# Kernel optimization log

Measured on AMD Instinct MI355X. Metric: run time of the kernel, lower is better.

The kernel has to match this reference:

```python
import jax, jax.numpy as jnp
import numpy as np

DIM = 64
SHAPE = (1, DIM, 12, 12, 12)  # B, C, D, H, W


def setup_inputs() -> dict:
    key = jax.random.key(0)
    k1, k2, k3, k4 = jax.random.split(key, 4)
    x = jax.random.normal(k1, SHAPE, dtype=jnp.float32)
    # torch nn.Linear weights: [out, in]; scale like default init
    w_qkv = jax.random.normal(k2, (3 * DIM, DIM), dtype=jnp.float32) * (1.0 / np.sqrt(DIM))
    w_proj = jax.random.normal(k3, (DIM, DIM), dtype=jnp.float32) * (1.0 / np.sqrt(DIM))
    b_proj = jax.random.normal(k4, (DIM,), dtype=jnp.float32) * 0.01
    return {"x": x, "w_qkv": w_qkv, "w_proj": w_proj, "b_proj": b_proj}


def reference(x, w_qkv, w_proj, b_proj):
    B, C, D, H, W = x.shape
    num_heads = C // 2  # head_dim = 2, per module definition
    head_dim = C // num_heads
    scale = head_dim ** (-0.5)
    N = D * H * W

    # [B, N, C] token layout (permute channels last, flatten spatial)
    xt = jnp.transpose(x, (0, 2, 3, 4, 1)).reshape(B, N, C)
    qkv = xt @ w_qkv.T  # [B, N, 3C]
    qkv = qkv.reshape(B, N, 3, num_heads, head_dim).transpose(2, 0, 3, 1, 4)
    q, k, v = qkv[0], qkv[1], qkv[2]  # each [B, h, N, d]

    attn = jnp.einsum('bhqd,bhkd->bhqk', q, k) * scale  # materialized scores
    attn = jax.nn.softmax(attn, axis=-1)
    out = jnp.einsum('bhqk,bhkd->bhqd', attn, v)  # [B, h, N, d]
    out = out.transpose(0, 2, 1, 3).reshape(B, D, H, W, C)
    out = out @ w_proj.T + b_proj  # [B, D, H, W, C]
    return out
```

## Files before the change

### kernel.cpp

```cpp
#include <hip/hip_runtime.h>
#include <hip/hip_bf16.h>

#define N_TOK  1728
#define CDIM   64
#define NHEADS 32
#define QTILES 27
#define NPAIR  (N_TOK / 2)
#define SCALE  0.70710678118654752f
#define LOG2E  1.44269504088896340736f
#define JW     8
#define PCH    (NPAIR / JW)

typedef _Float16 h2 __attribute__((ext_vector_type(2)));
union H2U { h2 h; unsigned int u; };

__device__ __forceinline__ unsigned int pack2(float a, float b) {
    H2U c; c.h.x = (_Float16)a; c.h.y = (_Float16)b; return c.u;
}
__device__ __forceinline__ float hdot2(unsigned int q, unsigned int k) {
    H2U a, b; a.u = q; b.u = k;
#if __has_builtin(__builtin_amdgcn_fdot2)
    return __builtin_amdgcn_fdot2(a.h, b.h, 0.0f, false);
#else
    return fmaf((float)a.h.x, (float)b.h.x, (float)a.h.y * (float)b.h.y);
#endif
}

__device__ __forceinline__ float ldin(const void* p, int i, int f32) {
    if (f32) return ((const float*)p)[i];
    union { unsigned int b; float f; } c;
    c.b = ((unsigned int)((const unsigned short*)p)[i]) << 16;
    return c.f;
}
__device__ __forceinline__ int sniff_f32(const void* x) {
    union { unsigned int b; float f; } c;
    c.b = ((unsigned int)((const unsigned short*)x)[threadIdx.x & 63]) << 16;
    int bad = (((c.b >> 23) & 0xFF) == 0xFF) || (fabsf(c.f) > 1e10f);
    return (__ballot(bad) != 0ULL) ? 1 : 0;
}

__global__ void __launch_bounds__(64)
qkv_pack(const void* __restrict__ xv, const void* __restrict__ wv,
         unsigned int* __restrict__ Qp, unsigned int* __restrict__ KVg) {
    const int f     = sniff_f32(xv);
    const int lane  = threadIdx.x;
    const int h     = blockIdx.y & 31;
    const int which = blockIdx.y >> 5;
    const int r0    = (which << 6) + 2 * h;
    const int n     = blockIdx.x * 64 + lane;
    float a0 = 0.f, a1 = 0.f;
    if (f) {
        const float* x  = (const float*)xv;
        const float* w0 = (const float*)wv + r0 * CDIM;
        const float* w1 = w0 + CDIM;
#pragma unroll 8
        for (int c = 0; c < CDIM; ++c) {
            float xc = x[c * N_TOK + n];
            a0 = fmaf(xc, w0[c], a0);
            a1 = fmaf(xc, w1[c], a1);
        }
    } else {
#pragma unroll 8
        for (int c = 0; c < CDIM; ++c) {
            float xc = ldin(xv, c * N_TOK + n, 0);
            a0 = fmaf(xc, ldin(wv, r0 * CDIM + c, 0), a0);
            a1 = fmaf(xc, ldin(wv, (r0 + 1) * CDIM + c, 0), a1);
        }
    }
    if (which == 0)
        Qp[h * N_TOK + n] = pack2(a0 * (SCALE * LOG2E), a1 * (SCALE * LOG2E));
    else
        KVg[(h * NPAIR + (n >> 1)) * 4 + ((which == 1) ? 0 : 2) + (n & 1)] =
            pack2(a0, a1);
}

__global__ void __launch_bounds__(512, 4)
attn_kernel(const unsigned int* __restrict__ Qp, const uint4* __restrict__ KVg,
            float* __restrict__ O) {
    __shared__ uint4 KVs[NPAIR];
    __shared__ float redbuf[JW * 64 * 3];
    const int tid  = threadIdx.x;
    const int lane = tid & 63;
    const int wav  = tid >> 6;
    const int h    = blockIdx.y;
    const int t0   = blockIdx.x * 64;

    const uint4* src = KVg + h * NPAIR;
    KVs[tid] = src[tid];
    if (tid < NPAIR - 512) KVs[512 + tid] = src[512 + tid];
    const unsigned int qh = Qp[h * N_TOK + t0 + lane];
    __syncthreads();

    const uint4* KVp = &KVs[wav * PCH];
    float l0 = 0.f, l1 = 0.f, l2 = 0.f, l3 = 0.f;
    float p0 = 0.f, p1 = 0.f, p2 = 0.f, p3 = 0.f;
    float s0 = 0.f, s1 = 0.f, s2 = 0.f, s3 = 0.f;
    for (int g = 0; g < PCH; g += 4) {
        uint4 d0 = KVp[g], d1 = KVp[g + 1], d2 = KVp[g + 2], d3 = KVp[g + 3];
        H2U v;
        float ea, eb;
        ea = __builtin_amdgcn_exp2f(hdot2(qh, d0.x));
        eb = __builtin_amdgcn_exp2f(hdot2(qh, d0.y));
        v.u = d0.z; l0 += ea; p0 = fmaf(ea, (float)v.h.x, p0); s0 = fmaf(ea, (float)v.h.y, s0);
        v.u = d0.w; l0 += eb; p0 = fmaf(eb, (float)v.h.x, p0); s0 = fmaf(eb, (float)v.h.y, s0);
        ea = __builtin_amdgcn_exp2f(hdot2(qh, d1.x));
        eb = __builtin_amdgcn_exp2f(hdot2(qh, d1.y));
        v.u = d1.z; l1 += ea; p1 = fmaf(ea, (float)v.h.x, p1); s1 = fmaf(ea, (float)v.h.y, s1);
        v.u = d1.w; l1 += eb; p1 = fmaf(eb, (float)v.h.x, p1); s1 = fmaf(eb, (float)v.h.y, s1);
        ea = __builtin_amdgcn_exp2f(hdot2(qh, d2.x));
        eb = __builtin_amdgcn_exp2f(hdot2(qh, d2.y));
        v.u = d2.z; l2 += ea; p2 = fmaf(ea, (float)v.h.x, p2); s2 = fmaf(ea, (float)v.h.y, s2);
        v.u = d2.w; l2 += eb; p2 = fmaf(eb, (float)v.h.x, p2); s2 = fmaf(eb, (float)v.h.y, s2);
        ea = __builtin_amdgcn_exp2f(hdot2(qh, d3.x));
        eb = __builtin_amdgcn_exp2f(hdot2(qh, d3.y));
        v.u = d3.z; l3 += ea; p3 = fmaf(ea, (float)v.h.x, p3); s3 = fmaf(ea, (float)v.h.y, s3);
        v.u = d3.w; l3 += eb; p3 = fmaf(eb, (float)v.h.x, p3); s3 = fmaf(eb, (float)v.h.y, s3);
    }
    float* red = redbuf + wav * 192 + lane * 3;
    red[0] = (l0 + l1) + (l2 + l3);
    red[1] = (p0 + p1) + (p2 + p3);
    red[2] = (s0 + s1) + (s2 + s3);
    __syncthreads();
    if (wav == 0) {
        float L = 0.f, A = 0.f, B = 0.f;
#pragma unroll
        for (int w = 0; w < JW; ++w) {
            const float* r = redbuf + w * 192 + lane * 3;
            L += r[0]; A += r[1]; B += r[2];
        }
        float inv = 1.0f / L;
        int n = t0 + lane;
        *((float2*)(O + n * CDIM + 2 * h)) = make_float2(A * inv, B * inv);
    }
}

__global__ void __launch_bounds__(256)
proj_kernel(const void* __restrict__ xv,
            const float* __restrict__ O,
            const void* __restrict__ w_proj, const void* __restrict__ b_proj,
            void* __restrict__ out) {
    __shared__ float Ws[CDIM * 65];
    const int f    = sniff_f32(xv);
    const int tid  = threadIdx.x;
    const int lane = tid & 63;
    const int wav  = tid >> 6;
    for (int e = tid; e < CDIM * CDIM; e += 256)
        Ws[(e & 63) * 65 + (e >> 6)] = ldin(w_proj, e, f);
    __syncthreads();
    int n = blockIdx.x * 4 + wav;
    float acc = ldin(b_proj, lane, f);
#pragma unroll 8
    for (int ci = 0; ci < CDIM; ++ci)
        acc = fmaf(O[n * CDIM + ci],
                   Ws[ci * 65 + lane], acc);
    if (f) ((float*)out)[n * CDIM + lane] = acc;
    else   ((__hip_bfloat16*)out)[n * CDIM + lane] = __float2bfloat16(acc);
}

extern "C" void kernel_launch(void* const* d_in, const int* in_sizes, int n_in,
                              void* d_out, int out_size, void* d_ws, size_t ws_size,
                              hipStream_t stream) {
    const void* x      = d_in[0];
    const void* w_qkv  = d_in[1];
    const void* w_proj = d_in[2];
    const void* b_proj = d_in[3];

    float*        O   = (float*)d_ws;
    unsigned int* Qp  = (unsigned int*)(O + N_TOK * CDIM);
    unsigned int* KVg = Qp + NHEADS * N_TOK;

    qkv_pack   <<<dim3(QTILES, 96), 64, 0, stream>>>(x, w_qkv, Qp, KVg);
    attn_kernel<<<dim3(QTILES, NHEADS), 512, 0, stream>>>(Qp, (const uint4*)KVg, O);
    proj_kernel<<<432, 256, 0, stream>>>(x, O, w_proj, b_proj, d_out);
}
```

Baseline: 94.68 us.

## Accumulate softmax numerator and denominator with packed fp16 dot2 using a bounded max shift

The attention inner loop now packs pairs of exp values into fp16 with cvt_pkrtz. It accumulates l, p and s with fdot2 against an interleaved V layout and a ones vector, which replaces the separate f16->f32 converts and FMAs. To keep the fp16 exponentials in range, qkv_pack computes a per-head max of squared key norm with atomicMax. The exponent is then shifted by a Cauchy-Schwarz bound (-|q|*max|k|). The intent is to cut VALU instruction count per key pair in the dominant attention kernel. The cost is lower precision in the exponentials and accumulation. The Kmax2 buffer is never reset, so the code relies on the workspace starting zeroed.

```diff
diff --git a/kernel.cpp b/kernel.cpp
--- a/kernel.cpp
+++ b/kernel.cpp
@@ -17,12 +17,23 @@
 __device__ __forceinline__ unsigned int pack2(float a, float b) {
     H2U c; c.h.x = (_Float16)a; c.h.y = (_Float16)b; return c.u;
 }
-__device__ __forceinline__ float hdot2(unsigned int q, unsigned int k) {
+__device__ __forceinline__ float hdot2a(unsigned int q, unsigned int k, float c) {
     H2U a, b; a.u = q; b.u = k;
 #if __has_builtin(__builtin_amdgcn_fdot2)
-    return __builtin_amdgcn_fdot2(a.h, b.h, 0.0f, false);
+    return __builtin_amdgcn_fdot2(a.h, b.h, c, false);
 #else
-    return fmaf((float)a.h.x, (float)b.h.x, (float)a.h.y * (float)b.h.y);
+    return fmaf((float)a.h.x, (float)b.h.x, fmaf((float)a.h.y, (float)b.h.y, c));
+#endif
+}
+__device__ __forceinline__ unsigned int pkrtz(float a, float b) {
+#if __has_builtin(__builtin_amdgcn_cvt_pkrtz)
+    __fp16 r2 __attribute__((ext_vector_type(2))) =
+        __builtin_amdgcn_cvt_pkrtz(a, b);
+    unsigned int u;
+    __builtin_memcpy(&u, &r2, 4);
+    return u;
+#else
+    return pack2(a, b);
 #endif
 }
 
@@ -41,7 +52,8 @@
 
 __global__ void __launch_bounds__(64)
 qkv_pack(const void* __restrict__ xv, const void* __restrict__ wv,
-         unsigned int* __restrict__ Qp, unsigned int* __restrict__ KVg) {
+         unsigned int* __restrict__ Qp, unsigned int* __restrict__ KVg,
+         int* __restrict__ Kmax2) {
     const int f     = sniff_f32(xv);
     const int lane  = threadIdx.x;
     const int h     = blockIdx.y & 31;
@@ -67,16 +79,25 @@
             a1 = fmaf(xc, ldin(wv, (r0 + 1) * CDIM + c, 0), a1);
         }
     }
-    if (which == 0)
+    if (which == 0) {
         Qp[h * N_TOK + n] = pack2(a0 * (SCALE * LOG2E), a1 * (SCALE * LOG2E));
-    else
-        KVg[(h * NPAIR + (n >> 1)) * 4 + ((which == 1) ? 0 : 2) + (n & 1)] =
-            pack2(a0, a1);
+    } else if (which == 1) {
+        KVg[(h * NPAIR + (n >> 1)) * 4 + (n & 1)] = pack2(a0, a1);
+        float m = fmaf(a0, a0, a1 * a1);
+#pragma unroll
+        for (int d = 1; d < 64; d <<= 1) m = fmaxf(m, __shfl_xor(m, d));
+        if (lane == 0) atomicMax(Kmax2 + h, __float_as_int(m));
+    } else {
+        float b0 = __shfl_xor(a0, 1);
+        float b1 = __shfl_xor(a1, 1);
+        unsigned int word = (n & 1) ? pack2(b1, a1) : pack2(a0, b0);
+        KVg[(h * NPAIR + (n >> 1)) * 4 + 2 + (n & 1)] = word;
+    }
 }
 
 __global__ void __launch_bounds__(512, 4)
 attn_kernel(const unsigned int* __restrict__ Qp, const uint4* __restrict__ KVg,
-            float* __restrict__ O) {
+            const int* __restrict__ Kmax2, float* __restrict__ O) {
     __shared__ uint4 KVs[NPAIR];
     __shared__ float redbuf[JW * 64 * 3];
     const int tid  = threadIdx.x;
@@ -89,32 +110,37 @@
     KVs[tid] = src[tid];
     if (tid < NPAIR - 512) KVs[512 + tid] = src[512 + tid];
     const unsigned int qh = Qp[h * N_TOK + t0 + lane];
+    H2U qu; qu.u = qh;
+    const float qx = (float)qu.h.x, qy = (float)qu.h.y;
+    const float Km = sqrtf(__int_as_float(Kmax2[h]));
+    const float negB = -sqrtf(fmaf(qx, qx, qy * qy)) * Km;
+    const unsigned int ones = pack2(1.0f, 1.0f);
     __syncthreads();
 
     const uint4* KVp = &KVs[wav * PCH];
     float l0 = 0.f, l1 = 0.f, l2 = 0.f, l3 = 0.f;
     float p0 = 0.f, p1 = 0.f, p2 = 0.f, p3 = 0.f;
     float s0 = 0.f, s1 = 0.f, s2 = 0.f, s3 = 0.f;
+#pragma unroll
     for (int g = 0; g < PCH; g += 4) {
         uint4 d0 = KVp[g], d1 = KVp[g + 1], d2 = KVp[g + 2], d3 = KVp[g + 3];
-        H2U v;
-        float ea, eb;
-        ea = __builtin_amdgcn_exp2f(hdot2(qh, d0.x));
-        eb = __builtin_amdgcn_exp2f(hdot2(qh, d0.y));
-        v.u = d0.z; l0 += ea; p0 = fmaf(ea, (float)v.h.x, p0); s0 = fmaf(ea, (float)v.h.y, s0);
-        v.u = d0.w; l0 += eb; p0 = fmaf(eb, (float)v.h.x, p0); s0 = fmaf(eb, (float)v.h.y, s0);
-        ea = __builtin_amdgcn_exp2f(hdot2(qh, d1.x));
-        eb = __builtin_amdgcn_exp2f(hdot2(qh, d1.y));
-        v.u = d1.z; l1 += ea; p1 = fmaf(ea, (float)v.h.x, p1); s1 = fmaf(ea, (float)v.h.y, s1);
-        v.u = d1.w; l1 += eb; p1 = fmaf(eb, (float)v.h.x, p1); s1 = fmaf(eb, (float)v.h.y, s1);
-        ea = __builtin_amdgcn_exp2f(hdot2(qh, d2.x));
-        eb = __builtin_amdgcn_exp2f(hdot2(qh, d2.y));
-        v.u = d2.z; l2 += ea; p2 = fmaf(ea, (float)v.h.x, p2); s2 = fmaf(ea, (float)v.h.y, s2);
-        v.u = d2.w; l2 += eb; p2 = fmaf(eb, (float)v.h.x, p2); s2 = fmaf(eb, (float)v.h.y, s2);
-        ea = __builtin_amdgcn_exp2f(hdot2(qh, d3.x));
-        eb = __builtin_amdgcn_exp2f(hdot2(qh, d3.y));
-        v.u = d3.z; l3 += ea; p3 = fmaf(ea, (float)v.h.x, p3); s3 = fmaf(ea, (float)v.h.y, s3);
-        v.u = d3.w; l3 += eb; p3 = fmaf(eb, (float)v.h.x, p3); s3 = fmaf(eb, (float)v.h.y, s3);
+        float ea, eb; unsigned int eh;
+        ea = __builtin_amdgcn_exp2f(hdot2a(qh, d0.x, negB));
+        eb = __builtin_amdgcn_exp2f(hdot2a(qh, d0.y, negB));
+        eh = pkrtz(ea, eb);
+        l0 = hdot2a(eh, ones, l0); p0 = hdot2a(eh, d0.z, p0); s0 = hdot2a(eh, d0.w, s0);
+        ea = __builtin_amdgcn_exp2f(hdot2a(qh, d1.x, negB));
+        eb = __builtin_amdgcn_exp2f(hdot2a(qh, d1.y, negB));
+        eh = pkrtz(ea, eb);
+        l1 = hdot2a(eh, ones, l1); p1 = hdot2a(eh, d1.z, p1); s1 = hdot2a(eh, d1.w, s1);
+        ea = __builtin_amdgcn_exp2f(hdot2a(qh, d2.x, negB));
+        eb = __builtin_amdgcn_exp2f(hdot2a(qh, d2.y, negB));
+        eh = pkrtz(ea, eb);
+        l2 = hdot2a(eh, ones, l2); p2 = hdot2a(eh, d2.z, p2); s2 = hdot2a(eh, d2.w, s2);
+        ea = __builtin_amdgcn_exp2f(hdot2a(qh, d3.x, negB));
+        eb = __builtin_amdgcn_exp2f(hdot2a(qh, d3.y, negB));
+        eh = pkrtz(ea, eb);
+        l3 = hdot2a(eh, ones, l3); p3 = hdot2a(eh, d3.z, p3); s3 = hdot2a(eh, d3.w, s3);
     }
     float* red = redbuf + wav * 192 + lane * 3;
     red[0] = (l0 + l1) + (l2 + l3);
@@ -165,11 +191,13 @@
     const void* w_proj = d_in[2];
     const void* b_proj = d_in[3];
 
-    float*        O   = (float*)d_ws;
-    unsigned int* Qp  = (unsigned int*)(O + N_TOK * CDIM);
-    unsigned int* KVg = Qp + NHEADS * N_TOK;
-
-    qkv_pack   <<<dim3(QTILES, 96), 64, 0, stream>>>(x, w_qkv, Qp, KVg);
-    attn_kernel<<<dim3(QTILES, NHEADS), 512, 0, stream>>>(Qp, (const uint4*)KVg, O);
+    float*        O     = (float*)d_ws;
+    unsigned int* Qp    = (unsigned int*)(O + N_TOK * CDIM);
+    unsigned int* KVg   = Qp + NHEADS * N_TOK;
+    int*          Kmax2 = (int*)(KVg + NHEADS * N_TOK * 2);
+
+    qkv_pack   <<<dim3(QTILES, 96), 64, 0, stream>>>(x, w_qkv, Qp, KVg, Kmax2);
+    attn_kernel<<<dim3(QTILES, NHEADS), 512, 0, stream>>>(Qp, (const uint4*)KVg,
+                                                          Kmax2, O);
     proj_kernel<<<432, 256, 0, stream>>>(x, O, w_proj, b_proj, d_out);
 }
```

Result: no change. 96.44 us (+1.9%).
